# Performance work log

Measured on AMD Instinct MI355X. Metric: run time of the kernel, lower is better.

The kernel has to match this reference:

```python
import jax, jax.numpy as jnp
import numpy as np

N, D, E = 16384, 2048, 64   # tokens, d_model, num_experts
K = 9                        # self.k = min(k+1, num_experts) with k=8
EPS = 0.01
SIGMA = 1.0 / E              # Normal(0, 1/num_experts) stddev


def setup_inputs() -> dict:
    key = jax.random.key(0)
    ks = jax.random.split(key, 6)
    x = jax.random.normal(ks[0], (N, D), jnp.float32)
    Wr = jax.random.normal(ks[1], (D, E), jnp.float32) * 0.02
    br = jnp.zeros((E,), jnp.float32)
    Wn = jax.random.normal(ks[2], (D, E), jnp.float32) * 0.02
    bn = jnp.zeros((E,), jnp.float32)
    noise_eps = jax.random.normal(ks[3], (N, E), jnp.float32)
    # torch: (-empty.exponential_()).log() -> log of Exp(1) samples
    gumbel_noise = jnp.log(jax.random.exponential(ks[4], (N, E), jnp.float32))
    return {"x": x, "Wr": Wr, "br": br, "Wn": Wn, "bn": bn,
            "noise_eps": noise_eps, "gumbel_noise": gumbel_noise}


def reference(x, Wr, br, Wn, bn, noise_eps, gumbel_noise):
    raw_logits = x @ Wr + br                              # [N, E]
    noise_stddev = jax.nn.softplus(x @ Wn + bn) + EPS     # [N, E]
    noisy_logits = raw_logits + noise_eps * noise_stddev  # [N, E]

    top_vals, top_idx = jax.lax.top_k(noisy_logits, K)    # [N, K] sorted desc
    # scatter ones at top-k indices (indices unique per row)
    hard_mask = jax.nn.one_hot(top_idx, E, dtype=noisy_logits.dtype).sum(axis=1)  # [N, E]

    # gumbel-softmax straight-through relaxation
    mask_soft = jax.nn.softmax(noisy_logits + gumbel_noise, axis=-1)
    expert_mask = hard_mask - jax.lax.stop_gradient(mask_soft) + mask_soft

    route_prob = jax.nn.softmax(noisy_logits, axis=-1)    # [N, E]
    importance = jax.nn.softmax(raw_logits, axis=-1).sum(axis=0)  # [E]

    # load: P(raw + noise > threshold), Normal(0, 1/E) CDF per original
    threshold = top_vals[:, K - 1]                        # [N]
    z = (threshold[:, None] - raw_logits) / noise_stddev  # [N, E]
    cdf = 0.5 * (1.0 + jax.scipy.special.erf(z / (SIGMA * jnp.sqrt(jnp.float32(2.0)))))
    load = (1.0 - cdf).sum(axis=0)                        # [E]

    return (expert_mask, route_prob, importance, load)
```

## Files before the change

kernel.cpp:

```cpp
#include <hip/hip_runtime.h>
#include <hip/hip_bf16.h>
#include <math.h>

#define N_TOK 16384
#define DIM   2048
#define NE    64
#define TOPK  9

#define ROWS     64
#define DC       64
#define NCHUNK   (DIM / DC)
#define NTHREADS 256

typedef short  short8  __attribute__((ext_vector_type(8)));
typedef float  float4_ __attribute__((ext_vector_type(4)));
typedef unsigned short ushort_t;

#define BUF_F 12288

__device__ __forceinline__ void async16(const void* g, void* l) {
    __builtin_amdgcn_global_load_lds(
        (const __attribute__((address_space(1))) void*)g,
        (__attribute__((address_space(3))) void*)l, 16, 0, 0);
}

__device__ __forceinline__ unsigned pk2(float a, float b) {
    float2 f; f.x = a; f.y = b;
    __hip_bfloat162 h = __float22bfloat162_rn(f);
    unsigned u;
    __builtin_memcpy(&u, &h, 4);
    return u;
}

__device__ __forceinline__ void cvt8(const float4_ va, const float4_ vb,
                                     short8* h, short8* l) {
    union { short8 s; unsigned u[4]; } H, L;
    const float f[8] = {va[0], va[1], va[2], va[3], vb[0], vb[1], vb[2], vb[3]};
#pragma unroll
    for (int i = 0; i < 4; ++i) {
        const float a = f[2 * i], b = f[2 * i + 1];
        const unsigned p = pk2(a, b);
        H.u[i] = p;
        const float ha = __uint_as_float(p << 16);
        const float hb = __uint_as_float(p & 0xffff0000u);
        L.u[i] = pk2(a - ha, b - hb);
    }
    *h = H.s; *l = L.s;
}

__device__ __forceinline__ float wave_max64(float v) {
#pragma unroll
    for (int off = 32; off > 0; off >>= 1)
        v = fmaxf(v, __shfl_xor(v, off, 64));
    return v;
}
__device__ __forceinline__ float wave_sum64(float v) {
#pragma unroll
    for (int off = 32; off > 0; off >>= 1)
        v += __shfl_xor(v, off, 64);
    return v;
}

__global__ __launch_bounds__(256)
void prep_w(const float* __restrict__ Wr, const float* __restrict__ Wn,
            ushort_t* __restrict__ wsW)
{
    const int gid = blockIdx.x * 256 + threadIdx.x;
    const int j  = gid & 7;
    const int l  = (gid >> 3) & 63;
    const int ct = (gid >> 9) & 7;
    const int kc = gid >> 12;
    const int k  = kc * 32 + (l >> 4) * 8 + j;
    const int n  = ct * 16 + (l & 15);
    const float v = (n < NE) ? Wr[k * NE + n] : Wn[k * NE + (n - NE)];
    const unsigned uv = __float_as_uint(v);
    const unsigned hb = (uv + 0x7fffu + ((uv >> 16) & 1u)) & 0xffff0000u;
    const float lo = v - __uint_as_float(hb);
    const unsigned ul = __float_as_uint(lo);
    const unsigned lb = (ul + 0x7fffu + ((ul >> 16) & 1u)) >> 16;
    const size_t s0 = (size_t)(kc * 8 + ct) * 2;
    wsW[s0 * 512 + l * 8 + j]       = (ushort_t)(hb >> 16);
    wsW[(s0 + 1) * 512 + l * 8 + j] = (ushort_t)lb;
}

__global__ __launch_bounds__(NTHREADS, 1)
void moe_main(const float* __restrict__ x,
              const float* __restrict__ br,
              const float* __restrict__ bn,
              const float* __restrict__ noise_eps,
              const float* __restrict__ gumbel,
              const ushort_t* __restrict__ wsW,
              float* __restrict__ out)
{
    __shared__ __align__(16) float smem[2][BUF_F];

    const int t    = threadIdx.x;
    const int lane = t & 63;
    const int w    = t >> 6;
    const int c4   = lane & 15;
    const int q    = lane >> 4;
    const int row0 = blockIdx.x * ROWS;

    const float* gxp[4];
#pragma unroll
    for (int ii = 0; ii < 4; ++ii) {
        const int r  = 16 * w + 4 * ii + q;
        const int gk = c4 ^ (r & 15);
        gxp[ii] = x + (size_t)(row0 + r) * DIM + gk * 4;
    }
    const char* wsrc = (const char*)wsW + (size_t)(w * 8) * 1024 + lane * 16;

    int aoff[2][2];
#pragma unroll
    for (int kc = 0; kc < 2; ++kc) {
        const int g0 = kc * 8 + q * 2;
        aoff[kc][0] = c4 * 64 + ((g0 ^ c4) * 4);
        aoff[kc][1] = c4 * 64 + (((g0 + 1) ^ c4) * 4);
    }

    float4_ acc[4][2];
#pragma unroll
    for (int rt = 0; rt < 4; ++rt)
#pragma unroll
        for (int cc = 0; cc < 2; ++cc)
            acc[rt][cc] = (float4_)(0.f);

    {
        float* xb = &smem[0][0];
        char*  wb = (char*)&smem[0][4096];
#pragma unroll
        for (int ii = 0; ii < 4; ++ii) async16(gxp[ii], xb + (4 * w + ii) * 256);
#pragma unroll
        for (int jj = 0; jj < 8; ++jj) async16(wsrc + jj * 1024, wb + (w * 8 + jj) * 1024);
#pragma unroll
        for (int ii = 0; ii < 4; ++ii) gxp[ii] += DC;
        wsrc += 32 * 1024;
    }

    for (int ch = 0; ch < NCHUNK; ++ch) {
        __syncthreads();
        const int b = ch & 1;
        if (ch + 1 < NCHUNK) {
            float* xb = &smem[b ^ 1][0];
            char*  wb = (char*)&smem[b ^ 1][4096];
#pragma unroll
            for (int ii = 0; ii < 4; ++ii) async16(gxp[ii], xb + (4 * w + ii) * 256);
#pragma unroll
            for (int jj = 0; jj < 8; ++jj) async16(wsrc + jj * 1024, wb + (w * 8 + jj) * 1024);
#pragma unroll
            for (int ii = 0; ii < 4; ++ii) gxp[ii] += DC;
            wsrc += 32 * 1024;
        }
        const float* xb = &smem[b][0];
        const char*  wb = (const char*)&smem[b][4096];
#pragma unroll
        for (int kc = 0; kc < 2; ++kc) {
            short8 bhv[2], blv[2];
#pragma unroll
            for (int cc = 0; cc < 2; ++cc) {
                const int slot = (kc * 8 + (2 * w + cc)) * 2;
                bhv[cc] = *(const short8*)(wb + slot * 1024 + lane * 16);
                blv[cc] = *(const short8*)(wb + (slot + 1) * 1024 + lane * 16);
            }
#pragma unroll
            for (int rt = 0; rt < 4; ++rt) {
                const float4_ va = *(const float4_*)(xb + aoff[kc][0] + rt * 1024);
                const float4_ vb = *(const float4_*)(xb + aoff[kc][1] + rt * 1024);
                short8 ah, al;
                cvt8(va, vb, &ah, &al);
#pragma unroll
                for (int cc = 0; cc < 2; ++cc) {
                    acc[rt][cc] = __builtin_amdgcn_mfma_f32_16x16x32_bf16(ah, bhv[cc], acc[rt][cc], 0, 0, 0);
                    acc[rt][cc] = __builtin_amdgcn_mfma_f32_16x16x32_bf16(al, bhv[cc], acc[rt][cc], 0, 0, 0);
                    acc[rt][cc] = __builtin_amdgcn_mfma_f32_16x16x32_bf16(ah, blv[cc], acc[rt][cc], 0, 0, 0);
                }
            }
        }
    }

    float* rawS = &smem[0][0];
    float* noiS = &smem[0][4160];
#pragma unroll
    for (int rt = 0; rt < 4; ++rt)
#pragma unroll
        for (int cc = 0; cc < 2; ++cc) {
            const int colg = (2 * w + cc) * 16 + c4;
            float* basep = (colg < NE) ? rawS : noiS;
            const int col = colg & 63;
#pragma unroll
            for (int v = 0; v < 4; ++v) {
                const int row = rt * 16 + q * 4 + v;
                basep[row * 65 + col] = acc[rt][cc][v];
            }
        }
    __syncthreads();

    const float br_l = br[lane];
    const float bn_l = bn[lane];
    float imp_acc = 0.f, load_acc = 0.f;
    float* out_em   = out;
    float* out_rp   = out + (size_t)N_TOK * NE;
    float* out_imp  = out + (size_t)2 * N_TOK * NE;
    float* out_load = out_imp + NE;

#pragma unroll 1
    for (int r = 0; r < 16; ++r) {
        const int lrow = w * 16 + r;
        const int row  = row0 + lrow;
        const float raw = rawS[lrow * 65 + lane] + br_l;
        const float nl  = noiS[lrow * 65 + lane] + bn_l;
        const float sd = fmaxf(nl, 0.f) + log1pf(expf(-fabsf(nl))) + 0.01f;
        const float epsv = noise_eps[(size_t)row * NE + lane];
        const float gum  = gumbel  [(size_t)row * NE + lane];
        const float noisy = fmaf(epsv, sd, raw);

        float cur = noisy;
        float thr = 0.f, m0 = 0.f;
#pragma unroll 1
        for (int k = 0; k < TOPK; ++k) {
            const float m = wave_max64(cur);
            if (k == 0) m0 = m;
            thr = m;
            const unsigned long long bm = __ballot(cur == m);
            const int first = __ffsll(bm) - 1;
            if (lane == first) cur = -INFINITY;
        }
        const float hard = (noisy >= thr) ? 1.f : 0.f;

        const float g  = noisy + gum;
        const float eg = expf(g - wave_max64(g));
        const float ms = eg / wave_sum64(eg);
        const float em = (hard - ms) + ms;

        const float en = expf(noisy - m0);
        const float rp = en / wave_sum64(en);

        const float er = expf(raw - wave_max64(raw));
        imp_acc += er / wave_sum64(er);

        const float z = (thr - raw) / sd;
        load_acc += 0.5f * erfcf(z * 45.254833995939045f);

        out_em[(size_t)row * NE + lane] = em;
        out_rp[(size_t)row * NE + lane] = rp;
    }

    float* red = &smem[1][0];
    red[w * 64 + lane]       = imp_acc;
    red[256 + w * 64 + lane] = load_acc;
    __syncthreads();
    if (w == 0) {
        const float s1 = red[lane] + red[64 + lane] + red[128 + lane] + red[192 + lane];
        const float s2 = red[256 + lane] + red[320 + lane] + red[384 + lane] + red[448 + lane];
        atomicAdd(&out_imp[lane], s1);
        atomicAdd(&out_load[lane], s2);
    }
}

extern "C" void kernel_launch(void* const* d_in, const int* in_sizes, int n_in,
                              void* d_out, int out_size, void* d_ws, size_t ws_size,
                              hipStream_t stream)
{
    const float* x         = (const float*)d_in[0];
    const float* Wr        = (const float*)d_in[1];
    const float* br        = (const float*)d_in[2];
    const float* Wn        = (const float*)d_in[3];
    const float* bn        = (const float*)d_in[4];
    const float* noise_eps = (const float*)d_in[5];
    const float* gumbel    = (const float*)d_in[6];
    float* out = (float*)d_out;
    ushort_t* wsW = (ushort_t*)d_ws;

    (void)hipMemsetAsync((char*)d_out + (size_t)2 * N_TOK * NE * sizeof(float), 0,
                         2 * NE * sizeof(float), stream);
    prep_w<<<1024, 256, 0, stream>>>(Wr, Wn, wsW);
    moe_main<<<N_TOK / ROWS, NTHREADS, 0, stream>>>(
        x, br, bn, noise_eps, gumbel, wsW, out);
}
```

Before: 279.5 us.

## Halve row tile, read weights directly from global, raise occupancy

The row tile shrinks from 64 to 32 rows, and weight fragments are now read straight from global memory (L2-resident) into registers instead of being staged through LDS. LDS use drops to about 17 KB and launch bounds ask for 3 blocks per CU, which doubles the grid and is meant to improve latency hiding and load balance. prep_w now writes vectorised 16-byte stores with 8 elements per thread. In exchange, each block now re-reads the full weight matrix, doubling total weight traffic, and the global weight loads are issued synchronously inside the loop.

```diff
diff --git a/kernel.cpp b/kernel.cpp
--- a/kernel.cpp
+++ b/kernel.cpp
@@ -7,7 +7,7 @@
 #define NE    64
 #define TOPK  9
 
-#define ROWS     64
+#define ROWS     32
 #define DC       64
 #define NCHUNK   (DIM / DC)
 #define NTHREADS 256
@@ -15,8 +15,6 @@
 typedef short  short8  __attribute__((ext_vector_type(8)));
 typedef float  float4_ __attribute__((ext_vector_type(4)));
 typedef unsigned short ushort_t;
-
-#define BUF_F 12288
 
 __device__ __forceinline__ void async16(const void* g, void* l) {
     __builtin_amdgcn_global_load_lds(
@@ -66,24 +64,29 @@
             ushort_t* __restrict__ wsW)
 {
     const int gid = blockIdx.x * 256 + threadIdx.x;
-    const int j  = gid & 7;
-    const int l  = (gid >> 3) & 63;
-    const int ct = (gid >> 9) & 7;
-    const int kc = gid >> 12;
-    const int k  = kc * 32 + (l >> 4) * 8 + j;
-    const int n  = ct * 16 + (l & 15);
-    const float v = (n < NE) ? Wr[k * NE + n] : Wn[k * NE + (n - NE)];
-    const unsigned uv = __float_as_uint(v);
-    const unsigned hb = (uv + 0x7fffu + ((uv >> 16) & 1u)) & 0xffff0000u;
-    const float lo = v - __uint_as_float(hb);
-    const unsigned ul = __float_as_uint(lo);
-    const unsigned lb = (ul + 0x7fffu + ((ul >> 16) & 1u)) >> 16;
-    const size_t s0 = (size_t)(kc * 8 + ct) * 2;
-    wsW[s0 * 512 + l * 8 + j]       = (ushort_t)(hb >> 16);
-    wsW[(s0 + 1) * 512 + l * 8 + j] = (ushort_t)lb;
-}
-
-__global__ __launch_bounds__(NTHREADS, 1)
+    const int l   = gid & 63;
+    const int ct  = (gid >> 6) & 7;
+    const int kcg = gid >> 9;
+    const int n   = ct * 16 + (l & 15);
+    const int k0  = kcg * 32 + (l >> 4) * 8;
+    const float* src = (n < NE) ? (Wr + n) : (Wn + (n - NE));
+    union { short8 s; ushort_t us[8]; } H, L;
+#pragma unroll
+    for (int j = 0; j < 8; ++j) {
+        const float v = src[(size_t)(k0 + j) * NE];
+        const unsigned uv = __float_as_uint(v);
+        const unsigned hb = (uv + 0x7fffu + ((uv >> 16) & 1u)) & 0xffff0000u;
+        const float lo = v - __uint_as_float(hb);
+        const unsigned ul = __float_as_uint(lo);
+        H.us[j] = (ushort_t)(hb >> 16);
+        L.us[j] = (ushort_t)((ul + 0x7fffu + ((ul >> 16) & 1u)) >> 16);
+    }
+    const size_t s0 = (size_t)(kcg * 8 + ct) * 2;
+    *(short8*)(wsW + s0 * 512 + l * 8)         = H.s;
+    *(short8*)(wsW + (s0 + 1) * 512 + l * 8)   = L.s;
+}
+
+__global__ __launch_bounds__(NTHREADS, 3)
 void moe_main(const float* __restrict__ x,
               const float* __restrict__ br,
               const float* __restrict__ bn,
@@ -92,7 +95,7 @@
               const ushort_t* __restrict__ wsW,
               float* __restrict__ out)
 {
-    __shared__ __align__(16) float smem[2][BUF_F];
+    __shared__ __align__(16) float smem[4352];
 
     const int t    = threadIdx.x;
     const int lane = t & 63;
@@ -101,14 +104,16 @@
     const int q    = lane >> 4;
     const int row0 = blockIdx.x * ROWS;
 
-    const float* gxp[4];
-#pragma unroll
-    for (int ii = 0; ii < 4; ++ii) {
-        const int r  = 16 * w + 4 * ii + q;
+    const float* gxp[2];
+    int lxo[2];
+#pragma unroll
+    for (int ii = 0; ii < 2; ++ii) {
+        const int i  = 2 * w + ii;
+        const int r  = 4 * i + q;
         const int gk = c4 ^ (r & 15);
         gxp[ii] = x + (size_t)(row0 + r) * DIM + gk * 4;
-    }
-    const char* wsrc = (const char*)wsW + (size_t)(w * 8) * 1024 + lane * 16;
+        lxo[ii] = i * 256;
+    }
 
     int aoff[2][2];
 #pragma unroll
@@ -118,70 +123,60 @@
         aoff[kc][1] = c4 * 64 + (((g0 + 1) ^ c4) * 4);
     }
 
-    float4_ acc[4][2];
-#pragma unroll
-    for (int rt = 0; rt < 4; ++rt)
+    float4_ acc[2][2];
+#pragma unroll
+    for (int rt = 0; rt < 2; ++rt)
 #pragma unroll
         for (int cc = 0; cc < 2; ++cc)
             acc[rt][cc] = (float4_)(0.f);
 
-    {
-        float* xb = &smem[0][0];
-        char*  wb = (char*)&smem[0][4096];
-#pragma unroll
-        for (int ii = 0; ii < 4; ++ii) async16(gxp[ii], xb + (4 * w + ii) * 256);
-#pragma unroll
-        for (int jj = 0; jj < 8; ++jj) async16(wsrc + jj * 1024, wb + (w * 8 + jj) * 1024);
-#pragma unroll
-        for (int ii = 0; ii < 4; ++ii) gxp[ii] += DC;
-        wsrc += 32 * 1024;
-    }
+    const char* wsB = (const char*)wsW;
+
+#pragma unroll
+    for (int ii = 0; ii < 2; ++ii) { async16(gxp[ii], &smem[lxo[ii]]); gxp[ii] += DC; }
 
     for (int ch = 0; ch < NCHUNK; ++ch) {
         __syncthreads();
         const int b = ch & 1;
+        short8 bh[2][2], bl[2][2];
+#pragma unroll
+        for (int kc = 0; kc < 2; ++kc)
+#pragma unroll
+            for (int cc = 0; cc < 2; ++cc) {
+                const size_t off = (size_t)(((ch * 2 + kc) * 8) + 2 * w + cc) * 2048 + lane * 16;
+                bh[kc][cc] = *(const short8*)(wsB + off);
+                bl[kc][cc] = *(const short8*)(wsB + off + 1024);
+            }
         if (ch + 1 < NCHUNK) {
-            float* xb = &smem[b ^ 1][0];
-            char*  wb = (char*)&smem[b ^ 1][4096];
-#pragma unroll
-            for (int ii = 0; ii < 4; ++ii) async16(gxp[ii], xb + (4 * w + ii) * 256);
-#pragma unroll
-            for (int jj = 0; jj < 8; ++jj) async16(wsrc + jj * 1024, wb + (w * 8 + jj) * 1024);
-#pragma unroll
-            for (int ii = 0; ii < 4; ++ii) gxp[ii] += DC;
-            wsrc += 32 * 1024;
+#pragma unroll
+            for (int ii = 0; ii < 2; ++ii) {
+                async16(gxp[ii], &smem[(b ^ 1) * 2048 + lxo[ii]]);
+                gxp[ii] += DC;
+            }
         }
-        const float* xb = &smem[b][0];
-        const char*  wb = (const char*)&smem[b][4096];
-#pragma unroll
-        for (int kc = 0; kc < 2; ++kc) {
-            short8 bhv[2], blv[2];
-#pragma unroll
-            for (int cc = 0; cc < 2; ++cc) {
-                const int slot = (kc * 8 + (2 * w + cc)) * 2;
-                bhv[cc] = *(const short8*)(wb + slot * 1024 + lane * 16);
-                blv[cc] = *(const short8*)(wb + (slot + 1) * 1024 + lane * 16);
-            }
-#pragma unroll
-            for (int rt = 0; rt < 4; ++rt) {
-                const float4_ va = *(const float4_*)(xb + aoff[kc][0] + rt * 1024);
-                const float4_ vb = *(const float4_*)(xb + aoff[kc][1] + rt * 1024);
+        const float* xb = &smem[b * 2048];
+#pragma unroll
+        for (int kc = 0; kc < 2; ++kc)
+#pragma unroll
+            for (int rt = 0; rt < 2; ++rt) {
+                const float4_ va = *(const float4_*)(xb + rt * 1024 + aoff[kc][0]);
+                const float4_ vb = *(const float4_*)(xb + rt * 1024 + aoff[kc][1]);
                 short8 ah, al;
                 cvt8(va, vb, &ah, &al);
 #pragma unroll
                 for (int cc = 0; cc < 2; ++cc) {
-                    acc[rt][cc] = __builtin_amdgcn_mfma_f32_16x16x32_bf16(ah, bhv[cc], acc[rt][cc], 0, 0, 0);
-                    acc[rt][cc] = __builtin_amdgcn_mfma_f32_16x16x32_bf16(al, bhv[cc], acc[rt][cc], 0, 0, 0);
-                    acc[rt][cc] = __builtin_amdgcn_mfma_f32_16x16x32_bf16(ah, blv[cc], acc[rt][cc], 0, 0, 0);
+                    acc[rt][cc] = __builtin_amdgcn_mfma_f32_16x16x32_bf16(ah, bh[kc][cc], acc[rt][cc], 0, 0, 0);
+                    acc[rt][cc] = __builtin_amdgcn_mfma_f32_16x16x32_bf16(al, bh[kc][cc], acc[rt][cc], 0, 0, 0);
+                    acc[rt][cc] = __builtin_amdgcn_mfma_f32_16x16x32_bf16(ah, bl[kc][cc], acc[rt][cc], 0, 0, 0);
                 }
             }
-        }
-    }
-
-    float* rawS = &smem[0][0];
-    float* noiS = &smem[0][4160];
-#pragma unroll
-    for (int rt = 0; rt < 4; ++rt)
+    }
+
+    __syncthreads();
+    float* rawS = &smem[0];
+    float* noiS = &smem[2080];
+#pragma unroll
+    for (int rt = 0; rt < 2; ++rt)
 #pragma unroll
         for (int cc = 0; cc < 2; ++cc) {
             const int colg = (2 * w + cc) * 16 + c4;
@@ -204,8 +199,8 @@
     float* out_load = out_imp + NE;
 
 #pragma unroll 1
-    for (int r = 0; r < 16; ++r) {
-        const int lrow = w * 16 + r;
+    for (int r = 0; r < 8; ++r) {
+        const int lrow = w * 8 + r;
         const int row  = row0 + lrow;
         const float raw = rawS[lrow * 65 + lane] + br_l;
         const float nl  = noiS[lrow * 65 + lane] + bn_l;
@@ -245,13 +240,13 @@
         out_rp[(size_t)row * NE + lane] = rp;
     }
 
-    float* red = &smem[1][0];
-    red[w * 64 + lane]       = imp_acc;
-    red[256 + w * 64 + lane] = load_acc;
+    __syncthreads();
+    smem[w * 64 + lane]       = imp_acc;
+    smem[256 + w * 64 + lane] = load_acc;
     __syncthreads();
     if (w == 0) {
-        const float s1 = red[lane] + red[64 + lane] + red[128 + lane] + red[192 + lane];
-        const float s2 = red[256 + lane] + red[320 + lane] + red[384 + lane] + red[448 + lane];
+        const float s1 = smem[lane] + smem[64 + lane] + smem[128 + lane] + smem[192 + lane];
+        const float s2 = smem[256 + lane] + smem[320 + lane] + smem[384 + lane] + smem[448 + lane];
         atomicAdd(&out_imp[lane], s1);
         atomicAdd(&out_load[lane], s2);
     }
@@ -273,7 +268,7 @@
 
     (void)hipMemsetAsync((char*)d_out + (size_t)2 * N_TOK * NE * sizeof(float), 0,
                          2 * NE * sizeof(float), stream);
-    prep_w<<<1024, 256, 0, stream>>>(Wr, Wn, wsW);
+    prep_w<<<128, 256, 0, stream>>>(Wr, Wn, wsW);
     moe_main<<<N_TOK / ROWS, NTHREADS, 0, stream>>>(
         x, br, bn, noise_eps, gumbel, wsW, out);
 }
```

New measurement: 266.9 us. -4.5%, faster.
